# Optimization experiments

Hardware: AMD Instinct MI355X
Metric: run time of the kernel (lower is better)

## Reference

```python
import jax, jax.numpy as jnp
import numpy as np

H = W = 256          # input_img_height (square images)
N_NODES = 8          # camera graph nodes
N_EDGES = 64         # ~fully connected directed graph
FEAT = 1024          # edge_feat_dim
BN_EPS = 1e-5


def setup_inputs() -> dict:
    key = jax.random.key(0)
    ks = jax.random.split(key, 8)
    d = {}
    d["x"] = jax.random.normal(ks[0], (N_NODES, 3 * H * W), dtype=jnp.float32)
    d["edge_index"] = jax.random.randint(ks[1], (2, N_EDGES), 0, N_NODES)
    # ResNet stem params (conv1 replaced to take 6 channels)
    d["conv1_w"] = jax.random.normal(ks[2], (64, 6, 7, 7), dtype=jnp.float32) * 0.05
    d["bn_gamma"] = jnp.ones((64,), jnp.float32)
    d["bn_beta"] = jnp.zeros((64,), jnp.float32)
    d["bn_mean"] = jnp.zeros((64,), jnp.float32)
    d["bn_var"] = jnp.ones((64,), jnp.float32)
    d["fc_w"] = jax.random.normal(ks[3], (FEAT, 64), dtype=jnp.float32) * 0.05
    d["fc_b"] = jnp.zeros((FEAT,), jnp.float32)
    d["fc_xyz_w"] = jax.random.normal(ks[4], (3, FEAT), dtype=jnp.float32) * 0.05
    d["fc_xyz_b"] = jnp.zeros((3,), jnp.float32)
    d["fc_wpqr_w"] = jax.random.normal(ks[5], (3, FEAT), dtype=jnp.float32) * 0.05
    d["fc_wpqr_b"] = jnp.zeros((3,), jnp.float32)
    return d


def _edge_extractor(ef, conv1_w, bn_gamma, bn_beta, bn_mean, bn_var, fc_w, fc_b):
    # conv1: 6->64, 7x7, stride 2, pad 3, no bias
    y = jax.lax.conv_general_dilated(
        ef, conv1_w, window_strides=(2, 2), padding=[(3, 3), (3, 3)],
        dimension_numbers=("NCHW", "OIHW", "NCHW"))
    # BatchNorm (inference form with running stats), fused scale/shift
    scale = (bn_gamma * jax.lax.rsqrt(bn_var + BN_EPS))[None, :, None, None]
    shift = (bn_beta - bn_mean * bn_gamma * jax.lax.rsqrt(bn_var + BN_EPS))[None, :, None, None]
    y = jax.nn.relu(y * scale + shift)
    # maxpool 3x3 stride 2 pad 1
    y = jax.lax.reduce_window(y, -jnp.inf, jax.lax.max,
                              (1, 1, 3, 3), (1, 1, 2, 2),
                              [(0, 0), (0, 0), (1, 1), (1, 1)])
    # AdaptiveAvgPool2d(1) + fc to edge_feat_dim
    y = jnp.mean(y, axis=(2, 3))                     # [E, 64]
    return y @ fc_w.T + fc_b                         # [E, FEAT]


def reference(x, edge_index, conv1_w, bn_gamma, bn_beta, bn_mean, bn_var,
              fc_w, fc_b, fc_xyz_w, fc_xyz_b, fc_wpqr_w, fc_wpqr_b):
    imgs = x.reshape(N_NODES, 3, H, W)
    # compute_edge_features, vectorized: gather min/max node per edge, concat channels
    nmin = jnp.min(edge_index, axis=0)               # [E]
    nmax = jnp.max(edge_index, axis=0)               # [E]
    edge_feat = jnp.concatenate([imgs[nmin], imgs[nmax]], axis=1)  # [E, 6, H, W]
    ef = _edge_extractor(edge_feat, conv1_w, bn_gamma, bn_beta, bn_mean, bn_var, fc_w, fc_b)
    ef = jax.nn.relu(ef)
    # droprate == 0 -> no dropout
    xyz = ef @ fc_xyz_w.T + fc_xyz_b                 # [E, 3]
    wpqr = ef @ fc_wpqr_w.T + fc_wpqr_b              # [E, 3]
    full = jnp.concatenate([xyz, wpqr], axis=1)      # [E, 6]
    return (full[:N_NODES], full)
```

## Files before the change

kernel.cpp:

```cpp
#include <hip/hip_runtime.h>
#include <hip/hip_bf16.h>

#define N_NODES 8
#define N_EDGES 64
#define CO 64
#define OH 128
#define OW 128
#define FEAT 1024
#define BN_EPS 1e-5f

#define OFF_POOLED 0
#define OFF_WB     16384
#define OFF_SHIFT  65536
#define OFF_A      65792
#define OFF_B      (65792 + 16777216)

typedef short bf16x8 __attribute__((ext_vector_type(8)));
typedef float f32x4  __attribute__((ext_vector_type(4)));

__device__ __forceinline__ unsigned short f2bf(float f) {
    unsigned u = __float_as_uint(f);
    u += 0x7fffu + ((u >> 16) & 1u);
    return (unsigned short)(u >> 16);
}
__device__ __forceinline__ float blo(unsigned u) { return __uint_as_float(u << 16); }
__device__ __forceinline__ float bhi(unsigned u) { return __uint_as_float(u & 0xffff0000u); }

__global__ __launch_bounds__(256) void repack_kernel(
        const float* __restrict__ w,
        const float* __restrict__ gamma, const float* __restrict__ beta,
        const float* __restrict__ mean,  const float* __restrict__ var,
        unsigned short* __restrict__ wb2, float* __restrict__ shiftb,
        float* __restrict__ pooled) {
    int idx = blockIdx.x * 256 + threadIdx.x;
    if (idx < 2 * 64 * 192) {
        int t = idx % 192;
        int c = (idx / 192) & 63;
        int h = idx / (192 * 64);
        int rr = t >> 3, kx = t & 7;
        float val = 0.f;
        if (rr < 21 && kx < 7) {
            int ci = rr / 7, ky = rr % 7;
            float sc = gamma[c] * rsqrtf(var[c] + BN_EPS);
            val = w[((c * 6 + h * 3 + ci) * 7 + ky) * 7 + kx] * sc;
        }
        wb2[(rr * 128 + h * 64 + c) * 8 + kx] = f2bf(val);
    }
    if (idx < 64) {
        float sc = gamma[idx] * rsqrtf(var[idx] + BN_EPS);
        shiftb[idx] = beta[idx] - mean[idx] * sc;
    }
    if (idx < 64 * 64) pooled[idx] = 0.f;
}

#define RS_W 136

__global__ __launch_bounds__(512, 4) void conv_kernel(
        const float* __restrict__ x, const unsigned short* __restrict__ wb2,
        const float* __restrict__ shiftb,
        unsigned short* __restrict__ A2, unsigned short* __restrict__ B2) {
    int n  = blockIdx.x >> 7;
    int oy = blockIdx.x & 127;
    int t  = threadIdx.x;

    __shared__ __align__(16) char smem[62208];
    unsigned* rawu = (unsigned*)smem;
    uint4*    wl4  = (uint4*)(smem + 13056);

    for (int k = t; k < 3072; k += 512)
        wl4[k] = ((const uint4*)wb2)[k];

    const float* img = x + (size_t)n * (3 * 256 * 256);
    for (int k = t; k < 24 * RS_W; k += 512) {
        int u  = k % RS_W;
        int rr = k / RS_W;
        unsigned val = 0u;
        if (rr < 21 && u < 131) {
            int ci = (rr * 147) >> 10;
            int ky = rr - ci * 7;
            int iy = 2 * oy - 3 + ky;
            if ((unsigned)iy < 256u) {
                int c0 = 2 * u - 3;
                const float* row = img + (ci * 256 + iy) * 256;
                float f0 = ((unsigned)c0 < 256u) ? row[c0] : 0.f;
                float f1 = ((unsigned)(c0 + 1) < 256u) ? row[c0 + 1] : 0.f;
                val = (unsigned)f2bf(f0) | ((unsigned)f2bf(f1) << 16);
            }
        }
        rawu[k] = val;
    }
    __syncthreads();

    int wv = t >> 6, lane = t & 63;
    int h  = wv & 1, wg = wv >> 1;
    int quad = lane >> 4, m = lane & 15;

    f32x4 acc[4][2];
#pragma unroll
    for (int ct = 0; ct < 4; ++ct) {
        acc[ct][0] = (f32x4){0.f, 0.f, 0.f, 0.f};
        acc[ct][1] = (f32x4){0.f, 0.f, 0.f, 0.f};
    }

    const bf16x8* wlv = (const bf16x8*)(smem + 13056);

#pragma unroll
    for (int s = 0; s < 6; ++s) {
        int rq = 4 * s + quad;
        bf16x8 afrag[2];
#pragma unroll
        for (int nt = 0; nt < 2; ++nt) {
            int ox = 32 * wg + 16 * nt + m;
            int base = rq * RS_W + ox;
            union { unsigned u[4]; bf16x8 v; } bb;
            bb.u[0] = rawu[base];     bb.u[1] = rawu[base + 1];
            bb.u[2] = rawu[base + 2]; bb.u[3] = rawu[base + 3];
            afrag[nt] = bb.v;
        }
#pragma unroll
        for (int ct = 0; ct < 4; ++ct) {
            bf16x8 wfrag = wlv[rq * 128 + h * 64 + 16 * ct + m];
#pragma unroll
            for (int nt = 0; nt < 2; ++nt)
                acc[ct][nt] = __builtin_amdgcn_mfma_f32_16x16x32_bf16(
                                  afrag[nt], wfrag, acc[ct][nt], 0, 0, 0);
        }
    }

    float sh[4] = {0.f, 0.f, 0.f, 0.f};
    if (h) {
#pragma unroll
        for (int ct = 0; ct < 4; ++ct) sh[ct] = shiftb[16 * ct + m];
    }

    __syncthreads();
    unsigned short* T = (unsigned short*)smem;

#pragma unroll
    for (int ct = 0; ct < 4; ++ct) {
        int chp = h * 64 + 16 * ct + m;
#pragma unroll
        for (int nt = 0; nt < 2; ++nt) {
            int px0 = 32 * wg + 16 * nt + 4 * quad;
            float v0 = acc[ct][nt][0] + sh[ct];
            float v1 = acc[ct][nt][1] + sh[ct];
            float v2 = acc[ct][nt][2] + sh[ct];
            float v3 = acc[ct][nt][3] + sh[ct];
            uint2 pk;
            pk.x = (unsigned)f2bf(v0) | ((unsigned)f2bf(v1) << 16);
            pk.y = (unsigned)f2bf(v2) | ((unsigned)f2bf(v3) << 16);
            *(uint2*)&T[chp * 136 + px0] = pk;
        }
    }
    __syncthreads();

    int row = t >> 2, slot = t & 3;
    int hh = row >> 6, ch = row & 63;
    unsigned short* dst = (hh ? B2 : A2)
                        + ((size_t)(n * CO + ch) << 14) + (oy << 7) + slot * 32;
#pragma unroll
    for (int i = 0; i < 4; ++i)
        *(uint4*)(dst + i * 8) = *(uint4*)&T[row * 136 + slot * 32 + i * 8];
}

__global__ __launch_bounds__(256) void pool_kernel(
        const int* __restrict__ ei,
        const unsigned short* __restrict__ A2,
        const unsigned short* __restrict__ B2,
        float* __restrict__ pooled) {
    int b  = blockIdx.x;
    int c  = b >> 4;
    int rt = b & 15;
    int t  = threadIdx.x;

    __shared__ unsigned short S[2 * 8 * 9 * 128];

    for (int k = t; k < 2304; k += 256) {
        int slot = k & 15;
        int r    = (k >> 4) % 9;
        int tn   = (k >> 4) / 9;
        int grow = 8 * rt - 1 + r;
        uint4 v = make_uint4(0u, 0u, 0u, 0u);
        if (grow >= 0) {
            const unsigned short* src = (tn >= 8) ? B2 : A2;
            int node = tn & 7;
            v = *(const uint4*)(src + ((size_t)(node * CO + c) << 14)
                                    + (grow << 7) + slot * 8);
        }
        *(uint4*)&S[tn * 1152 + (r << 7) + slot * 8] = v;
    }
    __syncthreads();

    int wv = t >> 6, lane = t & 63;
    int esub = lane >> 4, tc = lane & 15;

    for (int i = 0; i < 4; ++i) {
        int e = 16 * wv + 4 * i + esub;
        int a0 = ei[e], a1 = ei[N_EDGES + e];
        int nmin = min(a0, a1), nmax = max(a0, a1);
        const unsigned short* pa = &S[nmin * 1152];
        const unsigned short* pb = &S[(8 + nmax) * 1152];

        float mx[4][4];
#pragma unroll
        for (int p = 0; p < 4; ++p)
#pragma unroll
            for (int q = 0; q < 4; ++q) mx[p][q] = 0.f;

#pragma unroll
        for (int r = 0; r < 9; ++r) {
            uint4 ga = *(const uint4*)(pa + (r << 7) + tc * 8);
            uint4 gb = *(const uint4*)(pb + (r << 7) + tc * 8);
            float ha = 0.f, hb = 0.f;
            if (tc > 0) {
                ha = bhi(*(const unsigned*)(pa + (r << 7) + tc * 8 - 2));
                hb = bhi(*(const unsigned*)(pb + (r << 7) + tc * 8 - 2));
            }
            float z0 = ha + hb;
            float z1 = blo(ga.x) + blo(gb.x), z2 = bhi(ga.x) + bhi(gb.x);
            float z3 = blo(ga.y) + blo(gb.y), z4 = bhi(ga.y) + bhi(gb.y);
            float z5 = blo(ga.z) + blo(gb.z), z6 = bhi(ga.z) + bhi(gb.z);
            float z7 = blo(ga.w) + blo(gb.w), z8 = bhi(ga.w) + bhi(gb.w);
            float h0 = fmaxf(fmaxf(z0, z1), z2);
            float h1 = fmaxf(fmaxf(z2, z3), z4);
            float h2 = fmaxf(fmaxf(z4, z5), z6);
            float h3 = fmaxf(fmaxf(z6, z7), z8);
            if (r & 1) {
                int p = (r - 1) >> 1;
                mx[p][0] = fmaxf(mx[p][0], h0); mx[p][1] = fmaxf(mx[p][1], h1);
                mx[p][2] = fmaxf(mx[p][2], h2); mx[p][3] = fmaxf(mx[p][3], h3);
            } else {
                if (r >= 2) {
                    int p = (r >> 1) - 1;
                    mx[p][0] = fmaxf(mx[p][0], h0); mx[p][1] = fmaxf(mx[p][1], h1);
                    mx[p][2] = fmaxf(mx[p][2], h2); mx[p][3] = fmaxf(mx[p][3], h3);
                }
                if (r <= 6) {
                    int p = r >> 1;
                    mx[p][0] = fmaxf(mx[p][0], h0); mx[p][1] = fmaxf(mx[p][1], h1);
                    mx[p][2] = fmaxf(mx[p][2], h2); mx[p][3] = fmaxf(mx[p][3], h3);
                }
            }
        }

        float sum = 0.f;
#pragma unroll
        for (int p = 0; p < 4; ++p)
#pragma unroll
            for (int q = 0; q < 4; ++q) sum += fmaxf(mx[p][q], 0.f);

        sum += __shfl_down(sum, 8, 64);
        sum += __shfl_down(sum, 4, 64);
        sum += __shfl_down(sum, 2, 64);
        sum += __shfl_down(sum, 1, 64);
        if (tc == 0) atomicAdd(&pooled[(e << 6) + c], sum);
    }
}

__global__ __launch_bounds__(256) void head_kernel(
        const float* __restrict__ pooled,
        const float* __restrict__ fc_w,   const float* __restrict__ fc_b,
        const float* __restrict__ xyz_w,  const float* __restrict__ xyz_b,
        const float* __restrict__ wpqr_w, const float* __restrict__ wpqr_b,
        float* __restrict__ out) {
    int e = blockIdx.x;
    int t = threadIdx.x;
    __shared__ float pl[CO];
    if (t < CO) pl[t] = pooled[(e << 6) + t] * (1.f / 4096.f);
    __syncthreads();

    float s[6] = {0.f, 0.f, 0.f, 0.f, 0.f, 0.f};
#pragma unroll
    for (int ff = 0; ff < 4; ++ff) {
        int f = ff * 256 + t;
        const float* wr = fc_w + f * CO;
        float d = fc_b[f];
#pragma unroll
        for (int c = 0; c < CO; ++c) d = fmaf(pl[c], wr[c], d);
        d = fmaxf(d, 0.f);
#pragma unroll
        for (int r = 0; r < 3; ++r) {
            s[r]     = fmaf(d, xyz_w[r * FEAT + f],  s[r]);
            s[3 + r] = fmaf(d, wpqr_w[r * FEAT + f], s[3 + r]);
        }
    }
#pragma unroll
    for (int r = 0; r < 6; ++r)
#pragma unroll
        for (int off = 32; off > 0; off >>= 1)
            s[r] += __shfl_down(s[r], off, 64);

    __shared__ float red[4][6];
    if ((t & 63) == 0) {
#pragma unroll
        for (int r = 0; r < 6; ++r) red[t >> 6][r] = s[r];
    }
    __syncthreads();
    if (t < 6) {
        float v = red[0][t] + red[1][t] + red[2][t] + red[3][t];
        v += (t < 3) ? xyz_b[t] : wpqr_b[t - 3];
        out[48 + e * 6 + t] = v;
        if (e < 8) out[e * 6 + t] = v;
    }
}

extern "C" void kernel_launch(void* const* d_in, const int* in_sizes, int n_in,
                              void* d_out, int out_size, void* d_ws, size_t ws_size,
                              hipStream_t stream) {
    const float* x        = (const float*)d_in[0];
    const int*   ei       = (const int*)d_in[1];
    const float* conv1_w  = (const float*)d_in[2];
    const float* bn_gamma = (const float*)d_in[3];
    const float* bn_beta  = (const float*)d_in[4];
    const float* bn_mean  = (const float*)d_in[5];
    const float* bn_var   = (const float*)d_in[6];
    const float* fc_w     = (const float*)d_in[7];
    const float* fc_b     = (const float*)d_in[8];
    const float* xyz_w    = (const float*)d_in[9];
    const float* xyz_b    = (const float*)d_in[10];
    const float* wpqr_w   = (const float*)d_in[11];
    const float* wpqr_b   = (const float*)d_in[12];
    float* out = (float*)d_out;

    char* ws = (char*)d_ws;
    float*          pooled = (float*)(ws + OFF_POOLED);
    unsigned short* wb2    = (unsigned short*)(ws + OFF_WB);
    float*          shiftb = (float*)(ws + OFF_SHIFT);
    unsigned short* A2     = (unsigned short*)(ws + OFF_A);
    unsigned short* B2     = (unsigned short*)(ws + OFF_B);

    repack_kernel<<<96, 256, 0, stream>>>(conv1_w, bn_gamma, bn_beta, bn_mean,
                                          bn_var, wb2, shiftb, pooled);
    conv_kernel<<<1024, 512, 0, stream>>>(x, wb2, shiftb, A2, B2);
    pool_kernel<<<1024, 256, 0, stream>>>(ei, A2, B2, pooled);
    head_kernel<<<64, 256, 0, stream>>>(pooled, fc_w, fc_b,
                                        xyz_w, xyz_b, wpqr_w, wpqr_b, out);
}
```

Measured before the change: 145.6 us.

## Pool over 36 unique node pairs and read conv weights from global

The pooling kernel now computes features for the 36 unordered (min,max) node pairs instead of all 64 edges, deduplicating repeated pairs. The head kernel maps each edge to its pair code when reading pooled features. Separately, the conv kernel drops the LDS staging of weights and loads weight fragments directly from global/L2, shrinking LDS to raise occupancy, and partially unrolls the tap loop. The direct loads risk higher latency per MFMA step, and pooled storage now assumes a 64-slot pair-code layout.

After: 137.8 us. 1.06x faster.

```diff
diff --git a/kernel.cpp b/kernel.cpp
--- a/kernel.cpp
+++ b/kernel.cpp
@@ -63,12 +63,8 @@
     int oy = blockIdx.x & 127;
     int t  = threadIdx.x;
 
-    __shared__ __align__(16) char smem[62208];
+    __shared__ __align__(16) char smem[34816];
     unsigned* rawu = (unsigned*)smem;
-    uint4*    wl4  = (uint4*)(smem + 13056);
-
-    for (int k = t; k < 3072; k += 512)
-        wl4[k] = ((const uint4*)wb2)[k];
 
     const float* img = x + (size_t)n * (3 * 256 * 256);
     for (int k = t; k < 24 * RS_W; k += 512) {
@@ -102,9 +98,9 @@
         acc[ct][1] = (f32x4){0.f, 0.f, 0.f, 0.f};
     }
 
-    const bf16x8* wlv = (const bf16x8*)(smem + 13056);
-
-#pragma unroll
+    const bf16x8* wbv = (const bf16x8*)wb2;
+
+#pragma unroll 2
     for (int s = 0; s < 6; ++s) {
         int rq = 4 * s + quad;
         bf16x8 afrag[2];
@@ -119,7 +115,7 @@
         }
 #pragma unroll
         for (int ct = 0; ct < 4; ++ct) {
-            bf16x8 wfrag = wlv[rq * 128 + h * 64 + 16 * ct + m];
+            bf16x8 wfrag = wbv[rq * 128 + h * 64 + 16 * ct + m];
 #pragma unroll
             for (int nt = 0; nt < 2; ++nt)
                 acc[ct][nt] = __builtin_amdgcn_mfma_f32_16x16x32_bf16(
@@ -163,8 +159,7 @@
         *(uint4*)(dst + i * 8) = *(uint4*)&T[row * 136 + slot * 32 + i * 8];
 }
 
-__global__ __launch_bounds__(256) void pool_kernel(
-        const int* __restrict__ ei,
+__global__ __launch_bounds__(256, 4) void pool_kernel(
         const unsigned short* __restrict__ A2,
         const unsigned short* __restrict__ B2,
         float* __restrict__ pooled) {
@@ -194,12 +189,15 @@
     int wv = t >> 6, lane = t & 63;
     int esub = lane >> 4, tc = lane & 15;
 
-    for (int i = 0; i < 4; ++i) {
-        int e = 16 * wv + 4 * i + esub;
-        int a0 = ei[e], a1 = ei[N_EDGES + e];
-        int nmin = min(a0, a1), nmax = max(a0, a1);
-        const unsigned short* pa = &S[nmin * 1152];
-        const unsigned short* pb = &S[(8 + nmax) * 1152];
+    for (int i = 0; i < 3; ++i) {
+        int sidx = 12 * wv + 4 * i + esub;
+        bool valid = sidx < 36;
+        int ss = valid ? sidx : 0;
+        int pi = 0, rem = ss;
+        while (rem >= 8 - pi) { rem -= 8 - pi; ++pi; }
+        int pj = pi + rem;
+        const unsigned short* pa = &S[pi * 1152];
+        const unsigned short* pb = &S[(8 + pj) * 1152];
 
         float mx[4][4];
 #pragma unroll
@@ -253,20 +251,23 @@
         sum += __shfl_down(sum, 4, 64);
         sum += __shfl_down(sum, 2, 64);
         sum += __shfl_down(sum, 1, 64);
-        if (tc == 0) atomicAdd(&pooled[(e << 6) + c], sum);
+        if (tc == 0 && valid)
+            atomicAdd(&pooled[((pi << 3) + pj) * 64 + c], sum);
     }
 }
 
 __global__ __launch_bounds__(256) void head_kernel(
-        const float* __restrict__ pooled,
+        const int* __restrict__ ei, const float* __restrict__ pooled,
         const float* __restrict__ fc_w,   const float* __restrict__ fc_b,
         const float* __restrict__ xyz_w,  const float* __restrict__ xyz_b,
         const float* __restrict__ wpqr_w, const float* __restrict__ wpqr_b,
         float* __restrict__ out) {
     int e = blockIdx.x;
     int t = threadIdx.x;
+    int a0 = ei[e], a1 = ei[N_EDGES + e];
+    int code = (min(a0, a1) << 3) + max(a0, a1);
     __shared__ float pl[CO];
-    if (t < CO) pl[t] = pooled[(e << 6) + t] * (1.f / 4096.f);
+    if (t < CO) pl[t] = pooled[(code << 6) + t] * (1.f / 4096.f);
     __syncthreads();
 
     float s[6] = {0.f, 0.f, 0.f, 0.f, 0.f, 0.f};
@@ -332,7 +333,7 @@
     repack_kernel<<<96, 256, 0, stream>>>(conv1_w, bn_gamma, bn_beta, bn_mean,
                                           bn_var, wb2, shiftb, pooled);
     conv_kernel<<<1024, 512, 0, stream>>>(x, wb2, shiftb, A2, B2);
-    pool_kernel<<<1024, 256, 0, stream>>>(ei, A2, B2, pooled);
-    head_kernel<<<64, 256, 0, stream>>>(pooled, fc_w, fc_b,
+    pool_kernel<<<1024, 256, 0, stream>>>(A2, B2, pooled);
+    head_kernel<<<64, 256, 0, stream>>>(ei, pooled, fc_w, fc_b,
                                         xyz_w, xyz_b, wpqr_w, wpqr_b, out);
 }
```
